# Kernel tuning notes

Measured on AMD Instinct MI355X. Metric: run time of the kernel, lower is better.

The kernel has to match this reference:

```python
import jax, jax.numpy as jnp
import numpy as np
import math

H = 2
NC, NPR = 100000, 50000
IN, HID, OUT = 128, 128, 16
E1, E2 = 300000, 300000
D = HID // H


def _segment_softmax(scores, seg, num_segments):
    m = jax.ops.segment_max(scores, seg, num_segments=num_segments)
    m = jax.lax.stop_gradient(jnp.where(jnp.isfinite(m), m, 0.0))
    e = jnp.exp(scores - m[seg])
    s = jax.ops.segment_sum(e, seg, num_segments=num_segments)
    return e / (s[seg] + 1e-16)


def _hgt_layer(xc, xp, ecp_s, ecp_d, epc_s, epc_d, prm):
    (wc, bc, wp, bp, acp, mcp, pcp, apc, mpc, ppc,
     owc, obc, owp, obp, sc, sp) = prm
    Nc, Np = xc.shape[0], xp.shape[0]

    def kqv(x, w, b):
        t = x @ w + b
        k, q, v = jnp.split(t, 3, axis=1)
        d = k.shape[1] // H
        return k.reshape(-1, H, d), q.reshape(-1, H, d), v.reshape(-1, H, d)

    kc, qc, vc = kqv(xc, wc, bc)
    kp, qp, vp = kqv(xp, wp, bp)
    d = kc.shape[-1]
    # relation-specific transforms applied to source-node keys/values (a_rel / m_rel)
    k_cp = jnp.einsum('nhd,hde->nhe', kc, acp)
    v_cp = jnp.einsum('nhd,hde->nhe', vc, mcp)
    k_pc = jnp.einsum('nhd,hde->nhe', kp, apc)
    v_pc = jnp.einsum('nhd,hde->nhe', vp, mpc)
    # merged destination index space: customers [0,Nc), products [Nc,Nc+Np)
    q_all = jnp.concatenate([qc, qp], axis=0)
    kj = jnp.concatenate([k_cp[ecp_s], k_pc[epc_s]], axis=0)  # [E,H,D] per-edge gather
    vj = jnp.concatenate([v_cp[ecp_s], v_pc[epc_s]], axis=0)
    dst = jnp.concatenate([ecp_d + Nc, epc_d], axis=0)
    prel = jnp.concatenate([jnp.broadcast_to(pcp, (ecp_s.shape[0], H)),
                            jnp.broadcast_to(ppc, (epc_s.shape[0], H))], axis=0)
    alpha = (q_all[dst] * kj).sum(-1) * prel / math.sqrt(d)  # [E,H]
    alpha = _segment_softmax(alpha, dst, Nc + Np)  # softmax over all incoming edges per dst node
    out = jax.ops.segment_sum(vj * alpha[..., None], dst, num_segments=Nc + Np)
    out = out.reshape(Nc + Np, H * d)

    def mix(o, x, ow, ob, s):
        o = jax.nn.gelu(o, approximate=False) @ ow + ob
        g = jax.nn.sigmoid(s)
        return g * o + (1.0 - g) * x

    return mix(out[:Nc], xc, owc, obc, sc), mix(out[Nc:], xp, owp, obp, sp)


def setup_inputs():
    key = jax.random.key(0)
    ks = list(jax.random.split(key, 64))
    it = iter(range(64))

    def nrm(shape, scale):
        return jax.random.normal(ks[next(it)], shape, dtype=jnp.float32) * scale

    inp = {}
    inp['xc'] = nrm((NC, IN), 1.0)
    inp['xp'] = nrm((NPR, IN), 1.0)
    for l in (1, 2):
        fin = IN if l == 1 else HID
        inp[f'w{l}c'] = nrm((fin, 3 * HID), 0.08)
        inp[f'b{l}c'] = jnp.zeros((3 * HID,), jnp.float32)
        inp[f'w{l}p'] = nrm((fin, 3 * HID), 0.08)
        inp[f'b{l}p'] = jnp.zeros((3 * HID,), jnp.float32)
        for et in ('cp', 'pc'):
            inp[f'a{l}{et}'] = nrm((H, D, D), 0.125)
            inp[f'm{l}{et}'] = nrm((H, D, D), 0.125)
            inp[f'p{l}{et}'] = jnp.ones((H,), jnp.float32)
        inp[f'ow{l}c'] = nrm((HID, HID), 0.08)
        inp[f'ob{l}c'] = jnp.zeros((HID,), jnp.float32)
        inp[f'ow{l}p'] = nrm((HID, HID), 0.08)
        inp[f'ob{l}p'] = jnp.zeros((HID,), jnp.float32)
        inp[f's{l}c'] = jnp.ones((1,), jnp.float32)
        inp[f's{l}p'] = jnp.ones((1,), jnp.float32)
    inp['wl'] = nrm((HID, OUT), 0.08)
    inp['bl'] = jnp.zeros((OUT,), jnp.float32)
    inp['ecp_s'] = jax.random.randint(ks[next(it)], (E1,), 0, NC, dtype=jnp.int32)
    inp['ecp_d'] = jax.random.randint(ks[next(it)], (E1,), 0, NPR, dtype=jnp.int32)
    inp['epc_s'] = jax.random.randint(ks[next(it)], (E2,), 0, NPR, dtype=jnp.int32)
    inp['epc_d'] = jax.random.randint(ks[next(it)], (E2,), 0, NC, dtype=jnp.int32)
    return inp


def reference(xc, xp, w1c, b1c, w1p, b1p, a1cp, m1cp, p1cp, a1pc, m1pc, p1pc, ow1c, ob1c, ow1p, ob1p, s1c, s1p, w2c, b2c, w2p, b2p, a2cp, m2cp, p2cp, a2pc, m2pc, p2pc, ow2c, ob2c, ow2p, ob2p, s2c, s2p, wl, bl, ecp_s, ecp_d, epc_s, epc_d):
    oc, op = _hgt_layer(xc, xp, ecp_s, ecp_d, epc_s, epc_d,
                        (w1c, b1c, w1p, b1p, a1cp, m1cp, p1cp, a1pc, m1pc, p1pc, ow1c, ob1c, ow1p, ob1p, s1c, s1p))
    oc, op = jax.nn.relu(oc), jax.nn.relu(op)
    oc, op = _hgt_layer(oc, op, ecp_s, ecp_d, epc_s, epc_d,
                        (w2c, b2c, w2p, b2p, a2cp, m2cp, p2cp, a2pc, m2pc, p2pc, ow2c, ob2c, ow2p, ob2p, s2c, s2p))
    return oc @ wl + bl
```

## Files before the change

### kernel.cpp

```cpp
#include <hip/hip_runtime.h>

typedef __attribute__((ext_vector_type(8))) short s16x8;
typedef __attribute__((ext_vector_type(4))) float f32x4;

constexpr int kNC = 100000;
constexpr int kNP = 50000;
constexpr int kNT = kNC + kNP;
constexpr int kE1 = 300000;
constexpr int kE2 = 300000;
constexpr int kCAP = 32;

__device__ __forceinline__ float geluf(float x) {
    return 0.5f * x * (1.0f + erff(x * 0.7071067811865475f));
}
__device__ __forceinline__ unsigned short f2bf(float f) {
    unsigned int u = __float_as_uint(f);
    u += 0x7fffu + ((u >> 16) & 1u);
    return (unsigned short)(u >> 16);
}
__device__ __forceinline__ float bf2f(unsigned short s) {
    return __uint_as_float(((unsigned int)s) << 16);
}

__global__ void fold_k(const float* __restrict__ w, const float* __restrict__ b,
                       const float* __restrict__ ar, const float* __restrict__ mr,
                       float* __restrict__ weff, float* __restrict__ beff) {
    int col = blockIdx.x;
    int i = threadIdx.x;
    float acc, bacc;
    if (col >= 128 && col < 256) {
        acc = w[i * 384 + col];
        bacc = b[col];
    } else {
        const float* rel = (col < 128) ? ar : mr;
        int base = (col < 128) ? 0 : 256;
        int c = col - base;
        int h = c >> 6, j = c & 63;
        acc = 0.0f; bacc = 0.0f;
        for (int d = 0; d < 64; ++d) {
            float rv = rel[(h * 64 + d) * 64 + j];
            acc  = fmaf(w[i * 384 + base + h * 64 + d], rv, acc);
            bacc = fmaf(b[base + h * 64 + d], rv, bacc);
        }
    }
    weff[i * 384 + col] = acc;
    if (i == 0) beff[col] = bacc;
}

struct Job {
    const float* W;
    const float* bias;
    const void* A;
    const float* Xres;
    const float* sgate;
    void* out;
    int M;
    int ldb;
    int abf16;
    int bf16out;
};

template<int PRO, int EPI, int RELU, int FINAL>
__global__ __launch_bounds__(256) void gemm128(
    Job j0, Job j1, Job j2, Job j3, Job j4, Job j5,
    const float* __restrict__ wl, const float* __restrict__ bl)
{
    Job J;
    switch (blockIdx.y) {
        case 0: J = j0; break;
        case 1: J = j1; break;
        case 2: J = j2; break;
        case 3: J = j3; break;
        case 4: J = j4; break;
        default: J = j5; break;
    }
    const int row0 = blockIdx.x * 128;
    if (row0 >= J.M) return;

    constexpr int LDE = 36;
    constexpr int LDP = 132;
    constexpr int NSM = FINAL ? (128 * LDP) : (2 * 128 * LDE);
    __shared__ unsigned short sm[NSM];
    unsigned short* As = sm;
    unsigned short* Bs = sm + 128 * LDE;

    const int t = threadIdx.x;
    const int lane = t & 63;
    const int w = t >> 6;
    const int l15 = lane & 15, l4 = lane >> 4;
    const int M = J.M;

    f32x4 acc[2][8];
    #pragma unroll
    for (int n = 0; n < 8; ++n) {
        float bv = J.bias[n * 16 + l15];
        acc[0][n] = f32x4{bv, bv, bv, bv};
        acc[1][n] = acc[0][n];
    }

    for (int kc = 0; kc < 4; ++kc) {
        const int k0 = kc * 32;
        uint2 pa[4];
        #pragma unroll
        for (int i = 0; i < 4; ++i) {
            int idx = i * 256 + t;
            int r = idx >> 3, kq = idx & 7;
            int gr = row0 + r;
            if (J.abf16) {
                ushort4 rv = {0, 0, 0, 0};
                if (gr < M) rv = *(const ushort4*)((const unsigned short*)J.A + (size_t)gr * 128 + k0 + kq * 4);
                if (PRO) {
                    pa[i].x = (unsigned)f2bf(geluf(bf2f(rv.x))) | ((unsigned)f2bf(geluf(bf2f(rv.y))) << 16);
                    pa[i].y = (unsigned)f2bf(geluf(bf2f(rv.z))) | ((unsigned)f2bf(geluf(bf2f(rv.w))) << 16);
                } else {
                    pa[i].x = (unsigned)rv.x | ((unsigned)rv.y << 16);
                    pa[i].y = (unsigned)rv.z | ((unsigned)rv.w << 16);
                }
            } else {
                float4 v = make_float4(0.f, 0.f, 0.f, 0.f);
                if (gr < M) v = *(const float4*)((const float*)J.A + (size_t)gr * 128 + k0 + kq * 4);
                if (PRO) { v.x = geluf(v.x); v.y = geluf(v.y); v.z = geluf(v.z); v.w = geluf(v.w); }
                pa[i].x = (unsigned)f2bf(v.x) | ((unsigned)f2bf(v.y) << 16);
                pa[i].y = (unsigned)f2bf(v.z) | ((unsigned)f2bf(v.w) << 16);
            }
        }
        float wv[4][4];
        #pragma unroll
        for (int i = 0; i < 4; ++i) {
            int idx = i * 256 + t;
            int c = idx & 127, kq = idx >> 7;
            #pragma unroll
            for (int k2 = 0; k2 < 4; ++k2)
                wv[i][k2] = J.W[(size_t)(k0 + kq * 4 + k2) * J.ldb + c];
        }
        if (kc) __syncthreads();
        #pragma unroll
        for (int i = 0; i < 4; ++i) {
            int idx = i * 256 + t;
            int r = idx >> 3, kq = idx & 7;
            *(uint2*)&As[r * LDE + kq * 4] = pa[i];
            int c = idx & 127, kq2 = idx >> 7;
            uint2 pb;
            pb.x = (unsigned)f2bf(wv[i][0]) | ((unsigned)f2bf(wv[i][1]) << 16);
            pb.y = (unsigned)f2bf(wv[i][2]) | ((unsigned)f2bf(wv[i][3]) << 16);
            *(uint2*)&Bs[c * LDE + kq2 * 4] = pb;
        }
        __syncthreads();

        union FR { uint2 u[2]; s16x8 v; };
        FR af[2];
        #pragma unroll
        for (int m = 0; m < 2; ++m) {
            const unsigned short* p = &As[(w * 32 + m * 16 + l15) * LDE + l4 * 4];
            af[m].u[0] = *(const uint2*)p;
            af[m].u[1] = *(const uint2*)(p + 16);
        }
        #pragma unroll
        for (int n = 0; n < 8; ++n) {
            const unsigned short* p = &Bs[(n * 16 + l15) * LDE + l4 * 4];
            FR bfr;
            bfr.u[0] = *(const uint2*)p;
            bfr.u[1] = *(const uint2*)(p + 16);
            acc[0][n] = __builtin_amdgcn_mfma_f32_16x16x32_bf16(af[0].v, bfr.v, acc[0][n], 0, 0, 0);
            acc[1][n] = __builtin_amdgcn_mfma_f32_16x16x32_bf16(af[1].v, bfr.v, acc[1][n], 0, 0, 0);
        }
    }

    float g = 0.f, omg = 0.f;
    if (EPI == 1) { g = 1.0f / (1.0f + expf(-J.sgate[0])); omg = 1.0f - g; }

    if (FINAL) __syncthreads();

    #pragma unroll
    for (int m = 0; m < 2; ++m) {
        #pragma unroll
        for (int r = 0; r < 4; ++r) {
            int lr = w * 32 + m * 16 + l4 * 4 + r;
            int gr = row0 + lr;
            bool ok = gr < M;
            #pragma unroll
            for (int n = 0; n < 8; ++n) {
                float v = acc[m][n][r];
                if (EPI == 1) {
                    float xv = ok ? J.Xres[(size_t)gr * 128 + n * 16 + l15] : 0.f;
                    v = g * v + omg * xv;
                    if (RELU) v = fmaxf(v, 0.0f);
                }
                if (FINAL) {
                    sm[lr * LDP + n * 16 + l15] = f2bf(v);
                } else if (ok) {
                    if (J.bf16out)
                        ((unsigned short*)J.out)[(size_t)gr * 128 + n * 16 + l15] = f2bf(v);
                    else
                        ((float*)J.out)[(size_t)gr * 128 + n * 16 + l15] = v;
                }
            }
        }
    }

    if (FINAL) {
        union FR { uint2 u[2]; s16x8 v; };
        f32x4 facc[2];
        float bv = bl[l15];
        facc[0] = f32x4{bv, bv, bv, bv};
        facc[1] = facc[0];
        #pragma unroll
        for (int kc2 = 0; kc2 < 4; ++kc2) {
            FR bfr;
            #pragma unroll
            for (int h = 0; h < 2; ++h) {
                float f0 = wl[(size_t)(kc2 * 32 + h * 16 + l4 * 4 + 0) * 16 + l15];
                float f1 = wl[(size_t)(kc2 * 32 + h * 16 + l4 * 4 + 1) * 16 + l15];
                float f2 = wl[(size_t)(kc2 * 32 + h * 16 + l4 * 4 + 2) * 16 + l15];
                float f3 = wl[(size_t)(kc2 * 32 + h * 16 + l4 * 4 + 3) * 16 + l15];
                bfr.u[h].x = (unsigned)f2bf(f0) | ((unsigned)f2bf(f1) << 16);
                bfr.u[h].y = (unsigned)f2bf(f2) | ((unsigned)f2bf(f3) << 16);
            }
            #pragma unroll
            for (int m = 0; m < 2; ++m) {
                FR afr;
                const unsigned short* p = &sm[(w * 32 + m * 16 + l15) * LDP + kc2 * 32 + l4 * 4];
                afr.u[0] = *(const uint2*)p;
                afr.u[1] = *(const uint2*)(p + 16);
                facc[m] = __builtin_amdgcn_mfma_f32_16x16x32_bf16(afr.v, bfr.v, facc[m], 0, 0, 0);
            }
        }
        #pragma unroll
        for (int m = 0; m < 2; ++m) {
            #pragma unroll
            for (int r = 0; r < 4; ++r) {
                int gr = row0 + w * 32 + m * 16 + l4 * 4 + r;
                if (gr < M) ((float*)J.out)[(size_t)gr * 16 + l15] = facc[m][r];
            }
        }
    }
}

__global__ __launch_bounds__(256) void build_bucket(
    const int* __restrict__ src, const int* __restrict__ dst, int E,
    int* __restrict__ cnt, int* __restrict__ bucket)
{
    int e = blockIdx.x * 256 + threadIdx.x;
    if (e >= E) return;
    int d = dst[e];
    int slot = atomicAdd(&cnt[d], 1);
    if (slot < kCAP) bucket[(size_t)d * kCAP + slot] = src[e];
}

__global__ __launch_bounds__(256) void fused_attn2(
    int nA, const int* __restrict__ cntA, const int* __restrict__ bucketA,
    const unsigned short* __restrict__ kA, const unsigned short* __restrict__ vA,
    unsigned short* __restrict__ qoA, const float* __restrict__ prelA,
    int nB, const int* __restrict__ cntB, const int* __restrict__ bucketB,
    const unsigned short* __restrict__ kB, const unsigned short* __restrict__ vB,
    unsigned short* __restrict__ qoB, const float* __restrict__ prelB)
{
    int wid = (blockIdx.x * 256 + threadIdx.x) >> 6;
    int lane = threadIdx.x & 63;
    const int* cnt; const int* bucket; const unsigned short* ks; const unsigned short* vs;
    unsigned short* qo; const float* prel;
    if (wid < nA) {
        cnt = cntA; bucket = bucketA; ks = kA; vs = vA; qo = qoA; prel = prelA;
    } else {
        wid -= nA;
        if (wid >= nB) return;
        cnt = cntB; bucket = bucketB; ks = kB; vs = vB; qo = qoB; prel = prelB;
    }
    int deg = cnt[wid];
    if (deg > kCAP) deg = kCAP;
    int mys = (lane < deg) ? bucket[(size_t)wid * kCAP + lane] : 0;
    unsigned int qv = *(const unsigned int*)(qo + (size_t)wid * 128 + lane * 2);
    float qx = bf2f((unsigned short)qv), qy = bf2f((unsigned short)(qv >> 16));
    float ph = prel[lane >> 5] * 0.125f;
    float m = -3.4e38f, ss = 0.f, o0 = 0.f, o1 = 0.f;
    for (int i = 0; i < deg; ++i) {
        int s = __shfl(mys, i);
        unsigned int kk = *(const unsigned int*)(ks + (size_t)s * 128 + lane * 2);
        float p = qx * bf2f((unsigned short)kk) + qy * bf2f((unsigned short)(kk >> 16));
        p += __shfl_xor(p, 1);
        p += __shfl_xor(p, 2);
        p += __shfl_xor(p, 4);
        p += __shfl_xor(p, 8);
        p += __shfl_xor(p, 16);
        float lg = p * ph;
        float mn = fmaxf(m, lg);
        float sc = __expf(m - mn);
        float wgt = __expf(lg - mn);
        unsigned int vv = *(const unsigned int*)(vs + (size_t)s * 128 + lane * 2);
        ss = ss * sc + wgt;
        o0 = o0 * sc + wgt * bf2f((unsigned short)vv);
        o1 = o1 * sc + wgt * bf2f((unsigned short)(vv >> 16));
        m = mn;
    }
    float r = 1.0f / (ss + 1e-16f);
    unsigned int ov = (unsigned)f2bf(o0 * r) | ((unsigned)f2bf(o1 * r) << 16);
    *(unsigned int*)(qo + (size_t)wid * 128 + lane * 2) = ov;
}

extern "C" void kernel_launch(void* const* d_in, const int* in_sizes, int n_in,
                              void* d_out, int out_size, void* d_ws, size_t ws_size,
                              hipStream_t stream)
{
    const float* xc  = (const float*)d_in[0];
    const float* xp  = (const float*)d_in[1];
    const float* w1c = (const float*)d_in[2];
    const float* b1c = (const float*)d_in[3];
    const float* w1p = (const float*)d_in[4];
    const float* b1p = (const float*)d_in[5];
    const float* a1cp= (const float*)d_in[6];
    const float* m1cp= (const float*)d_in[7];
    const float* p1cp= (const float*)d_in[8];
    const float* a1pc= (const float*)d_in[9];
    const float* m1pc= (const float*)d_in[10];
    const float* p1pc= (const float*)d_in[11];
    const float* ow1c= (const float*)d_in[12];
    const float* ob1c= (const float*)d_in[13];
    const float* ow1p= (const float*)d_in[14];
    const float* ob1p= (const float*)d_in[15];
    const float* s1c = (const float*)d_in[16];
    const float* s1p = (const float*)d_in[17];
    const float* w2c = (const float*)d_in[18];
    const float* b2c = (const float*)d_in[19];
    const float* w2p = (const float*)d_in[20];
    const float* b2p = (const float*)d_in[21];
    const float* a2pc= (const float*)d_in[25];
    const float* m2pc= (const float*)d_in[26];
    const float* p2pc= (const float*)d_in[27];
    const float* ow2c= (const float*)d_in[28];
    const float* ob2c= (const float*)d_in[29];
    const float* s2c = (const float*)d_in[32];
    const float* wl  = (const float*)d_in[34];
    const float* bl  = (const float*)d_in[35];
    const int* ecp_s = (const int*)d_in[36];
    const int* ecp_d = (const int*)d_in[37];
    const int* epc_s = (const int*)d_in[38];
    const int* epc_d = (const int*)d_in[39];
    float* outF = (float*)d_out;
    (void)in_sizes; (void)n_in; (void)out_size; (void)ws_size;

    char* ws = (char*)d_ws;
    size_t off = 0;
    auto take = [&](size_t bytes) { char* p = ws + off; off += (bytes + 255) & ~(size_t)255; return p; };
    char* R0 = take((size_t)kNC * 128 * 4);
    unsigned short* kC = (unsigned short*)R0;
    unsigned short* vC = (unsigned short*)(R0 + (size_t)kNC * 128 * 2);
    float* hc = (float*)R0;
    char* R1 = take((size_t)kNP * 128 * 4);
    unsigned short* kP = (unsigned short*)R1;
    unsigned short* vP = (unsigned short*)(R1 + (size_t)kNP * 128 * 2);
    unsigned short* kP2 = kP;
    unsigned short* vP2 = vP;
    unsigned short* qAll = (unsigned short*)take((size_t)kNT * 128 * 2);
    unsigned short* qC = qAll;
    unsigned short* qP = qAll + (size_t)kNC * 128;
    unsigned short* hp = (unsigned short*)take((size_t)kNP * 128 * 2);
    int* cntP = (int*)take((size_t)kNP * 4);
    int* cntC = (int*)take((size_t)kNC * 4);
    int* bucketP = (int*)take((size_t)kNP * kCAP * 4);
    int* bucketC = (int*)take((size_t)kNC * kCAP * 4);
    float* wec = (float*)take((size_t)128 * 384 * 4);
    float* bec = (float*)take((size_t)384 * 4);
    float* wep = (float*)take((size_t)128 * 384 * 4);
    float* bep = (float*)take((size_t)384 * 4);

    auto cdiv = [](int a, int b) { return (a + b - 1) / b; };
    dim3 blk(256);
    const int gx = cdiv(kNC, 128);
    const float* nf = nullptr;

    hipMemsetAsync(cntP, 0, (size_t)kNP * 4, stream);
    hipMemsetAsync(cntC, 0, (size_t)kNC * 4, stream);
    hipLaunchKernelGGL(build_bucket, dim3(cdiv(kE1, 256)), blk, 0, stream, ecp_s, ecp_d, kE1, cntP, bucketP);
    hipLaunchKernelGGL(build_bucket, dim3(cdiv(kE2, 256)), blk, 0, stream, epc_s, epc_d, kE2, cntC, bucketC);

    hipLaunchKernelGGL(fold_k, dim3(384), dim3(128), 0, stream, w1c, b1c, a1cp, m1cp, wec, bec);
    hipLaunchKernelGGL(fold_k, dim3(384), dim3(128), 0, stream, w1p, b1p, a1pc, m1pc, wep, bep);

    Job jkC = { wec + 0,   bec + 0,   xc, nf, nf, (void*)kC, kNC, 384, 0, 1 };
    Job jqC = { wec + 128, bec + 128, xc, nf, nf, (void*)qC, kNC, 384, 0, 1 };
    Job jvC = { wec + 256, bec + 256, xc, nf, nf, (void*)vC, kNC, 384, 0, 1 };
    Job jkP = { wep + 0,   bep + 0,   xp, nf, nf, (void*)kP, kNP, 384, 0, 1 };
    Job jqP = { wep + 128, bep + 128, xp, nf, nf, (void*)qP, kNP, 384, 0, 1 };
    Job jvP = { wep + 256, bep + 256, xp, nf, nf, (void*)vP, kNP, 384, 0, 1 };
    hipLaunchKernelGGL((gemm128<0,0,0,0>), dim3(gx, 6), blk, 0, stream,
                       jkC, jqC, jvC, jkP, jqP, jvP, nf, nf);

    hipLaunchKernelGGL(fused_attn2, dim3(cdiv(kNP + kNC, 4)), blk, 0, stream,
                       kNP, cntP, bucketP, kC, vC, qP, p1cp,
                       kNC, cntC, bucketC, kP, vP, qC, p1pc);

    Job jmC = { ow1c, ob1c, qC, xc, s1c, (void*)hc, kNC, 128, 1, 0 };
    Job jmP = { ow1p, ob1p, qP, xp, s1p, (void*)hp, kNP, 128, 1, 1 };
    hipLaunchKernelGGL((gemm128<1,1,1,0>), dim3(gx, 2), blk, 0, stream,
                       jmC, jmP, jmC, jmC, jmC, jmC, nf, nf);

    hipLaunchKernelGGL(fold_k, dim3(384), dim3(128), 0, stream, w2p, b2p, a2pc, m2pc, wep, bep);
    Job jk2 = { wep + 0,   bep + 0,   hp, nf, nf, (void*)kP2, kNP, 384, 1, 1 };
    Job jv2 = { wep + 256, bep + 256, hp, nf, nf, (void*)vP2, kNP, 384, 1, 1 };
    Job jq2 = { w2c + 128, b2c + 128, hc, nf, nf, (void*)qC,  kNC, 384, 0, 1 };
    hipLaunchKernelGGL((gemm128<0,0,0,0>), dim3(gx, 3), blk, 0, stream,
                       jk2, jv2, jq2, jk2, jk2, jk2, nf, nf);

    hipLaunchKernelGGL(fused_attn2, dim3(cdiv(kNC, 4)), blk, 0, stream,
                       kNC, cntC, bucketC, kP2, vP2, qC, p2pc,
                       0, cntC, bucketC, kP2, vP2, qC, p2pc);

    Job jf = { ow2c, ob2c, qC, hc, s2c, (void*)outF, kNC, 128, 1, 0 };
    hipLaunchKernelGGL((gemm128<1,1,0,1>), dim3(gx, 1), blk, 0, stream,
                       jf, jf, jf, jf, jf, jf, wl, bl);
}
```

Before: 434.8 us.

## Stage A tile once and compute K/Q/V outputs per block; two-pass softmax

The GEMM kernel now loads the full 128x128 A tile into shared memory once and loops over up to three weight matrices (K, Q, V) in the same block. Before, separate blocks per output each re-read and re-converted the input rows. Grids become 1D with per-job block offsets, so no blocks are launched for product jobs past their row count. The attention kernel swaps online-softmax rescaling for a two-pass scheme: logits are kept per lane, the max and sum are taken with shuffles, then a plain weighted accumulation runs. The cost is larger shared memory (about 73KB per block), which lowers occupancy, plus a serial weight load per output.

```diff
diff --git a/kernel.cpp b/kernel.cpp
--- a/kernel.cpp
+++ b/kernel.cpp
@@ -48,160 +48,146 @@
 }
 
 struct Job {
-    const float* W;
-    const float* bias;
     const void* A;
     const float* Xres;
     const float* sgate;
-    void* out;
-    int M;
-    int ldb;
-    int abf16;
-    int bf16out;
+    int M, ldb, abf16, nout, blk0;
+    const float* W0; const float* b0; void* out0; int bf0;
+    const float* W1; const float* b1; void* out1; int bf1;
+    const float* W2; const float* b2; void* out2; int bf2;
 };
 
-template<int PRO, int EPI, int RELU, int FINAL>
-__global__ __launch_bounds__(256) void gemm128(
-    Job j0, Job j1, Job j2, Job j3, Job j4, Job j5,
-    const float* __restrict__ wl, const float* __restrict__ bl)
+template<int PRO, int EPI, int RELU, int FINAL, int NJ>
+__global__ __launch_bounds__(256) void gemmN(
+    Job j0, Job j1, const float* __restrict__ wl, const float* __restrict__ blv)
 {
-    Job J;
-    switch (blockIdx.y) {
-        case 0: J = j0; break;
-        case 1: J = j1; break;
-        case 2: J = j2; break;
-        case 3: J = j3; break;
-        case 4: J = j4; break;
-        default: J = j5; break;
-    }
-    const int row0 = blockIdx.x * 128;
-    if (row0 >= J.M) return;
-
-    constexpr int LDE = 36;
-    constexpr int LDP = 132;
-    constexpr int NSM = FINAL ? (128 * LDP) : (2 * 128 * LDE);
-    __shared__ unsigned short sm[NSM];
-    unsigned short* As = sm;
-    unsigned short* Bs = sm + 128 * LDE;
+    Job J = j0;
+    if (NJ > 1 && (int)blockIdx.x >= j1.blk0) J = j1;
+    const int row0 = ((int)blockIdx.x - J.blk0) * 128;
+    const int M = J.M;
+    if (row0 >= M) return;
+
+    constexpr int CH = 128 * 36;
+    __shared__ unsigned short As[4 * CH];
+    __shared__ unsigned short Bs[4 * CH];
 
     const int t = threadIdx.x;
-    const int lane = t & 63;
-    const int w = t >> 6;
+    const int lane = t & 63, w = t >> 6;
     const int l15 = lane & 15, l4 = lane >> 4;
-    const int M = J.M;
-
-    f32x4 acc[2][8];
+
     #pragma unroll
-    for (int n = 0; n < 8; ++n) {
-        float bv = J.bias[n * 16 + l15];
-        acc[0][n] = f32x4{bv, bv, bv, bv};
-        acc[1][n] = acc[0][n];
-    }
-
-    for (int kc = 0; kc < 4; ++kc) {
-        const int k0 = kc * 32;
-        uint2 pa[4];
-        #pragma unroll
-        for (int i = 0; i < 4; ++i) {
-            int idx = i * 256 + t;
-            int r = idx >> 3, kq = idx & 7;
-            int gr = row0 + r;
-            if (J.abf16) {
-                ushort4 rv = {0, 0, 0, 0};
-                if (gr < M) rv = *(const ushort4*)((const unsigned short*)J.A + (size_t)gr * 128 + k0 + kq * 4);
-                if (PRO) {
-                    pa[i].x = (unsigned)f2bf(geluf(bf2f(rv.x))) | ((unsigned)f2bf(geluf(bf2f(rv.y))) << 16);
-                    pa[i].y = (unsigned)f2bf(geluf(bf2f(rv.z))) | ((unsigned)f2bf(geluf(bf2f(rv.w))) << 16);
-                } else {
-                    pa[i].x = (unsigned)rv.x | ((unsigned)rv.y << 16);
-                    pa[i].y = (unsigned)rv.z | ((unsigned)rv.w << 16);
+    for (int i = 0; i < 16; ++i) {
+        int q = i * 256 + t;
+        int kc = q >> 10, rem = q & 1023, r = rem >> 3, kq = rem & 7;
+        int gr = row0 + r;
+        uint2 pa;
+        if (J.abf16) {
+            ushort4 rv = {0, 0, 0, 0};
+            if (gr < M) rv = *(const ushort4*)((const unsigned short*)J.A + (size_t)gr * 128 + kc * 32 + kq * 4);
+            if (PRO) {
+                pa.x = (unsigned)f2bf(geluf(bf2f(rv.x))) | ((unsigned)f2bf(geluf(bf2f(rv.y))) << 16);
+                pa.y = (unsigned)f2bf(geluf(bf2f(rv.z))) | ((unsigned)f2bf(geluf(bf2f(rv.w))) << 16);
+            } else {
+                pa.x = (unsigned)rv.x | ((unsigned)rv.y << 16);
+                pa.y = (unsigned)rv.z | ((unsigned)rv.w << 16);
+            }
+        } else {
+            float4 v = make_float4(0.f, 0.f, 0.f, 0.f);
+            if (gr < M) v = *(const float4*)((const float*)J.A + (size_t)gr * 128 + kc * 32 + kq * 4);
+            if (PRO) { v.x = geluf(v.x); v.y = geluf(v.y); v.z = geluf(v.z); v.w = geluf(v.w); }
+            pa.x = (unsigned)f2bf(v.x) | ((unsigned)f2bf(v.y) << 16);
+            pa.y = (unsigned)f2bf(v.z) | ((unsigned)f2bf(v.w) << 16);
+        }
+        *(uint2*)&As[kc * CH + r * 36 + kq * 4] = pa;
+    }
+
+    float gg = 0.f, omg = 0.f;
+    if (EPI == 1) { gg = 1.0f / (1.0f + expf(-J.sgate[0])); omg = 1.0f - gg; }
+
+    union FR { uint2 u[2]; s16x8 v; };
+
+    #pragma unroll
+    for (int o = 0; o < 3; ++o) {
+        if (o >= J.nout) break;
+        const float* W  = (o == 0) ? J.W0 : (o == 1 ? J.W1 : J.W2);
+        const float* bi = (o == 0) ? J.b0 : (o == 1 ? J.b1 : J.b2);
+        void* outp      = (o == 0) ? J.out0 : (o == 1 ? J.out1 : J.out2);
+        const int bfo   = (o == 0) ? J.bf0 : (o == 1 ? J.bf1 : J.bf2);
+
+        if (o) __syncthreads();
+        #pragma unroll
+        for (int i = 0; i < 16; ++i) {
+            int q = i * 256 + t;
+            int kc = q >> 10, rem = q & 1023, kq = rem >> 7, c = rem & 127;
+            int kb = kc * 32 + kq * 4;
+            float f0 = W[(size_t)(kb + 0) * J.ldb + c];
+            float f1 = W[(size_t)(kb + 1) * J.ldb + c];
+            float f2 = W[(size_t)(kb + 2) * J.ldb + c];
+            float f3 = W[(size_t)(kb + 3) * J.ldb + c];
+            uint2 pb;
+            pb.x = (unsigned)f2bf(f0) | ((unsigned)f2bf(f1) << 16);
+            pb.y = (unsigned)f2bf(f2) | ((unsigned)f2bf(f3) << 16);
+            *(uint2*)&Bs[kc * CH + c * 36 + kq * 4] = pb;
+        }
+        __syncthreads();
+
+        f32x4 acc[2][8];
+        #pragma unroll
+        for (int n = 0; n < 8; ++n) {
+            float bv = bi[n * 16 + l15];
+            acc[0][n] = f32x4{bv, bv, bv, bv};
+            acc[1][n] = acc[0][n];
+        }
+        #pragma unroll
+        for (int kc = 0; kc < 4; ++kc) {
+            FR af[2];
+            #pragma unroll
+            for (int m = 0; m < 2; ++m) {
+                const unsigned short* p = &As[kc * CH + (w * 32 + m * 16 + l15) * 36 + l4 * 4];
+                af[m].u[0] = *(const uint2*)p;
+                af[m].u[1] = *(const uint2*)(p + 16);
+            }
+            #pragma unroll
+            for (int n = 0; n < 8; ++n) {
+                const unsigned short* p = &Bs[kc * CH + (n * 16 + l15) * 36 + l4 * 4];
+                FR bfr;
+                bfr.u[0] = *(const uint2*)p;
+                bfr.u[1] = *(const uint2*)(p + 16);
+                acc[0][n] = __builtin_amdgcn_mfma_f32_16x16x32_bf16(af[0].v, bfr.v, acc[0][n], 0, 0, 0);
+                acc[1][n] = __builtin_amdgcn_mfma_f32_16x16x32_bf16(af[1].v, bfr.v, acc[1][n], 0, 0, 0);
+            }
+        }
+
+        if (FINAL) __syncthreads();
+        #pragma unroll
+        for (int m = 0; m < 2; ++m) {
+            #pragma unroll
+            for (int r = 0; r < 4; ++r) {
+                int lr = w * 32 + m * 16 + l4 * 4 + r;
+                int gr = row0 + lr;
+                bool ok = gr < M;
+                #pragma unroll
+                for (int n = 0; n < 8; ++n) {
+                    float v = acc[m][n][r];
+                    if (EPI == 1) {
+                        float xv = ok ? J.Xres[(size_t)gr * 128 + n * 16 + l15] : 0.f;
+                        v = gg * v + omg * xv;
+                        if (RELU) v = fmaxf(v, 0.0f);
+                    }
+                    if (FINAL) {
+                        As[lr * 132 + n * 16 + l15] = f2bf(v);
+                    } else if (ok) {
+                        if (bfo) ((unsigned short*)outp)[(size_t)gr * 128 + n * 16 + l15] = f2bf(v);
+                        else     ((float*)outp)[(size_t)gr * 128 + n * 16 + l15] = v;
+                    }
                 }
-            } else {
-                float4 v = make_float4(0.f, 0.f, 0.f, 0.f);
-                if (gr < M) v = *(const float4*)((const float*)J.A + (size_t)gr * 128 + k0 + kq * 4);
-                if (PRO) { v.x = geluf(v.x); v.y = geluf(v.y); v.z = geluf(v.z); v.w = geluf(v.w); }
-                pa[i].x = (unsigned)f2bf(v.x) | ((unsigned)f2bf(v.y) << 16);
-                pa[i].y = (unsigned)f2bf(v.z) | ((unsigned)f2bf(v.w) << 16);
-            }
-        }
-        float wv[4][4];
-        #pragma unroll
-        for (int i = 0; i < 4; ++i) {
-            int idx = i * 256 + t;
-            int c = idx & 127, kq = idx >> 7;
-            #pragma unroll
-            for (int k2 = 0; k2 < 4; ++k2)
-                wv[i][k2] = J.W[(size_t)(k0 + kq * 4 + k2) * J.ldb + c];
-        }
-        if (kc) __syncthreads();
-        #pragma unroll
-        for (int i = 0; i < 4; ++i) {
-            int idx = i * 256 + t;
-            int r = idx >> 3, kq = idx & 7;
-            *(uint2*)&As[r * LDE + kq * 4] = pa[i];
-            int c = idx & 127, kq2 = idx >> 7;
-            uint2 pb;
-            pb.x = (unsigned)f2bf(wv[i][0]) | ((unsigned)f2bf(wv[i][1]) << 16);
-            pb.y = (unsigned)f2bf(wv[i][2]) | ((unsigned)f2bf(wv[i][3]) << 16);
-            *(uint2*)&Bs[c * LDE + kq2 * 4] = pb;
-        }
-        __syncthreads();
-
-        union FR { uint2 u[2]; s16x8 v; };
-        FR af[2];
-        #pragma unroll
-        for (int m = 0; m < 2; ++m) {
-            const unsigned short* p = &As[(w * 32 + m * 16 + l15) * LDE + l4 * 4];
-            af[m].u[0] = *(const uint2*)p;
-            af[m].u[1] = *(const uint2*)(p + 16);
-        }
-        #pragma unroll
-        for (int n = 0; n < 8; ++n) {
-            const unsigned short* p = &Bs[(n * 16 + l15) * LDE + l4 * 4];
-            FR bfr;
-            bfr.u[0] = *(const uint2*)p;
-            bfr.u[1] = *(const uint2*)(p + 16);
-            acc[0][n] = __builtin_amdgcn_mfma_f32_16x16x32_bf16(af[0].v, bfr.v, acc[0][n], 0, 0, 0);
-            acc[1][n] = __builtin_amdgcn_mfma_f32_16x16x32_bf16(af[1].v, bfr.v, acc[1][n], 0, 0, 0);
-        }
-    }
-
-    float g = 0.f, omg = 0.f;
-    if (EPI == 1) { g = 1.0f / (1.0f + expf(-J.sgate[0])); omg = 1.0f - g; }
-
-    if (FINAL) __syncthreads();
-
-    #pragma unroll
-    for (int m = 0; m < 2; ++m) {
-        #pragma unroll
-        for (int r = 0; r < 4; ++r) {
-            int lr = w * 32 + m * 16 + l4 * 4 + r;
-            int gr = row0 + lr;
-            bool ok = gr < M;
-            #pragma unroll
-            for (int n = 0; n < 8; ++n) {
-                float v = acc[m][n][r];
-                if (EPI == 1) {
-                    float xv = ok ? J.Xres[(size_t)gr * 128 + n * 16 + l15] : 0.f;
-                    v = g * v + omg * xv;
-                    if (RELU) v = fmaxf(v, 0.0f);
-                }
-                if (FINAL) {
-                    sm[lr * LDP + n * 16 + l15] = f2bf(v);
-                } else if (ok) {
-                    if (J.bf16out)
-                        ((unsigned short*)J.out)[(size_t)gr * 128 + n * 16 + l15] = f2bf(v);
-                    else
-                        ((float*)J.out)[(size_t)gr * 128 + n * 16 + l15] = v;
-                }
             }
         }
     }
 
     if (FINAL) {
-        union FR { uint2 u[2]; s16x8 v; };
         f32x4 facc[2];
-        float bv = bl[l15];
+        float bv = blv[l15];
         facc[0] = f32x4{bv, bv, bv, bv};
         facc[1] = facc[0];
         #pragma unroll
@@ -219,7 +205,7 @@
             #pragma unroll
             for (int m = 0; m < 2; ++m) {
                 FR afr;
-                const unsigned short* p = &sm[(w * 32 + m * 16 + l15) * LDP + kc2 * 32 + l4 * 4];
+                const unsigned short* p = &As[(w * 32 + m * 16 + l15) * 132 + kc2 * 32 + l4 * 4];
                 afr.u[0] = *(const uint2*)p;
                 afr.u[1] = *(const uint2*)(p + 16);
                 facc[m] = __builtin_amdgcn_mfma_f32_16x16x32_bf16(afr.v, bfr.v, facc[m], 0, 0, 0);
@@ -230,7 +216,7 @@
             #pragma unroll
             for (int r = 0; r < 4; ++r) {
                 int gr = row0 + w * 32 + m * 16 + l4 * 4 + r;
-                if (gr < M) ((float*)J.out)[(size_t)gr * 16 + l15] = facc[m][r];
+                if (gr < M) ((float*)J.out0)[(size_t)gr * 16 + l15] = facc[m][r];
             }
         }
     }
@@ -268,11 +254,13 @@
     }
     int deg = cnt[wid];
     if (deg > kCAP) deg = kCAP;
+    const int lane31 = lane & 31;
     int mys = (lane < deg) ? bucket[(size_t)wid * kCAP + lane] : 0;
     unsigned int qv = *(const unsigned int*)(qo + (size_t)wid * 128 + lane * 2);
     float qx = bf2f((unsigned short)qv), qy = bf2f((unsigned short)(qv >> 16));
     float ph = prel[lane >> 5] * 0.125f;
-    float m = -3.4e38f, ss = 0.f, o0 = 0.f, o1 = 0.f;
+
+    float mx = -3.4e38f, mylg = -3.4e38f;
     for (int i = 0; i < deg; ++i) {
         int s = __shfl(mys, i);
         unsigned int kk = *(const unsigned int*)(ks + (size_t)s * 128 + lane * 2);
@@ -283,17 +271,27 @@
         p += __shfl_xor(p, 8);
         p += __shfl_xor(p, 16);
         float lg = p * ph;
-        float mn = fmaxf(m, lg);
-        float sc = __expf(m - mn);
-        float wgt = __expf(lg - mn);
+        if (lane31 == i) mylg = lg;
+        mx = fmaxf(mx, lg);
+    }
+    float wgt = (lane31 < deg) ? __expf(mylg - mx) : 0.f;
+    float ssum = wgt;
+    ssum += __shfl_xor(ssum, 1);
+    ssum += __shfl_xor(ssum, 2);
+    ssum += __shfl_xor(ssum, 4);
+    ssum += __shfl_xor(ssum, 8);
+    ssum += __shfl_xor(ssum, 16);
+    float rr = 1.0f / (ssum + 1e-16f);
+
+    float o0 = 0.f, o1 = 0.f;
+    for (int i = 0; i < deg; ++i) {
+        int s = __shfl(mys, i);
+        float wi = __shfl(wgt, (lane & 32) + i);
         unsigned int vv = *(const unsigned int*)(vs + (size_t)s * 128 + lane * 2);
-        ss = ss * sc + wgt;
-        o0 = o0 * sc + wgt * bf2f((unsigned short)vv);
-        o1 = o1 * sc + wgt * bf2f((unsigned short)(vv >> 16));
-        m = mn;
-    }
-    float r = 1.0f / (ss + 1e-16f);
-    unsigned int ov = (unsigned)f2bf(o0 * r) | ((unsigned)f2bf(o1 * r) << 16);
+        o0 = fmaf(wi, bf2f((unsigned short)vv), o0);
+        o1 = fmaf(wi, bf2f((unsigned short)(vv >> 16)), o1);
+    }
+    unsigned int ov = (unsigned)f2bf(o0 * rr) | ((unsigned)f2bf(o1 * rr) << 16);
     *(unsigned int*)(qo + (size_t)wid * 128 + lane * 2) = ov;
 }
 
@@ -365,7 +363,8 @@
 
     auto cdiv = [](int a, int b) { return (a + b - 1) / b; };
     dim3 blk(256);
-    const int gx = cdiv(kNC, 128);
+    const int nbC = cdiv(kNC, 128);
+    const int nbP = cdiv(kNP, 128);
     const float* nf = nullptr;
 
     hipMemsetAsync(cntP, 0, (size_t)kNP * 4, stream);
@@ -376,36 +375,45 @@
     hipLaunchKernelGGL(fold_k, dim3(384), dim3(128), 0, stream, w1c, b1c, a1cp, m1cp, wec, bec);
     hipLaunchKernelGGL(fold_k, dim3(384), dim3(128), 0, stream, w1p, b1p, a1pc, m1pc, wep, bep);
 
-    Job jkC = { wec + 0,   bec + 0,   xc, nf, nf, (void*)kC, kNC, 384, 0, 1 };
-    Job jqC = { wec + 128, bec + 128, xc, nf, nf, (void*)qC, kNC, 384, 0, 1 };
-    Job jvC = { wec + 256, bec + 256, xc, nf, nf, (void*)vC, kNC, 384, 0, 1 };
-    Job jkP = { wep + 0,   bep + 0,   xp, nf, nf, (void*)kP, kNP, 384, 0, 1 };
-    Job jqP = { wep + 128, bep + 128, xp, nf, nf, (void*)qP, kNP, 384, 0, 1 };
-    Job jvP = { wep + 256, bep + 256, xp, nf, nf, (void*)vP, kNP, 384, 0, 1 };
-    hipLaunchKernelGGL((gemm128<0,0,0,0>), dim3(gx, 6), blk, 0, stream,
-                       jkC, jqC, jvC, jkP, jqP, jvP, nf, nf);
+    Job jC = { xc, nf, nf, kNC, 384, 0, 3, 0,
+               wec + 0,   bec + 0,   (void*)kC, 1,
+               wec + 128, bec + 128, (void*)qC, 1,
+               wec + 256, bec + 256, (void*)vC, 1 };
+    Job jP = { xp, nf, nf, kNP, 384, 0, 3, nbC,
+               wep + 0,   bep + 0,   (void*)kP, 1,
+               wep + 128, bep + 128, (void*)qP, 1,
+               wep + 256, bep + 256, (void*)vP, 1 };
+    hipLaunchKernelGGL((gemmN<0,0,0,0,2>), dim3(nbC + nbP), blk, 0, stream, jC, jP, nf, nf);
 
     hipLaunchKernelGGL(fused_attn2, dim3(cdiv(kNP + kNC, 4)), blk, 0, stream,
                        kNP, cntP, bucketP, kC, vC, qP, p1cp,
                        kNC, cntC, bucketC, kP, vP, qC, p1pc);
 
-    Job jmC = { ow1c, ob1c, qC, xc, s1c, (void*)hc, kNC, 128, 1, 0 };
-    Job jmP = { ow1p, ob1p, qP, xp, s1p, (void*)hp, kNP, 128, 1, 1 };
-    hipLaunchKernelGGL((gemm128<1,1,1,0>), dim3(gx, 2), blk, 0, stream,
-                       jmC, jmP, jmC, jmC, jmC, jmC, nf, nf);
+    Job mC = { qC, xc, s1c, kNC, 128, 1, 1, 0,
+               ow1c, ob1c, (void*)hc, 0,
+               nf, nf, nullptr, 0, nf, nf, nullptr, 0 };
+    Job mP = { qP, xp, s1p, kNP, 128, 1, 1, nbC,
+               ow1p, ob1p, (void*)hp, 1,
+               nf, nf, nullptr, 0, nf, nf, nullptr, 0 };
+    hipLaunchKernelGGL((gemmN<1,1,1,0,2>), dim3(nbC + nbP), blk, 0, stream, mC, mP, nf, nf);
 
     hipLaunchKernelGGL(fold_k, dim3(384), dim3(128), 0, stream, w2p, b2p, a2pc, m2pc, wep, bep);
-    Job jk2 = { wep + 0,   bep + 0,   hp, nf, nf, (void*)kP2, kNP, 384, 1, 1 };
-    Job jv2 = { wep + 256, bep + 256, hp, nf, nf, (void*)vP2, kNP, 384, 1, 1 };
-    Job jq2 = { w2c + 128, b2c + 128, hc, nf, nf, (void*)qC,  kNC, 384, 0, 1 };
-    hipLaunchKernelGGL((gemm128<0,0,0,0>), dim3(gx, 3), blk, 0, stream,
-                       jk2, jv2, jq2, jk2, jk2, jk2, nf, nf);
+
+    Job j2p = { hp, nf, nf, kNP, 384, 1, 2, 0,
+                wep + 0,   bep + 0,   (void*)kP2, 1,
+                wep + 256, bep + 256, (void*)vP2, 1,
+                nf, nf, nullptr, 0 };
+    Job j2c = { hc, nf, nf, kNC, 384, 0, 1, nbP,
+                w2c + 128, b2c + 128, (void*)qC, 1,
+                nf, nf, nullptr, 0, nf, nf, nullptr, 0 };
+    hipLaunchKernelGGL((gemmN<0,0,0,0,2>), dim3(nbP + nbC), blk, 0, stream, j2p, j2c, nf, nf);
 
     hipLaunchKernelGGL(fused_attn2, dim3(cdiv(kNC, 4)), blk, 0, stream,
                        kNC, cntC, bucketC, kP2, vP2, qC, p2pc,
                        0, cntC, bucketC, kP2, vP2, qC, p2pc);
 
-    Job jf = { ow2c, ob2c, qC, hc, s2c, (void*)outF, kNC, 128, 1, 0 };
-    hipLaunchKernelGGL((gemm128<1,1,0,1>), dim3(gx, 1), blk, 0, stream,
-                       jf, jf, jf, jf, jf, jf, wl, bl);
-}
+    Job jf = { qC, hc, s2c, kNC, 128, 1, 1, 0,
+               ow2c, ob2c, (void*)outF, 0,
+               nf, nf, nullptr, 0, nf, nf, nullptr, 0 };
+    hipLaunchKernelGGL((gemmN<1,1,0,1,1>), dim3(nbC), blk, 0, stream, jf, jf, wl, bl);
+}
```

New measurement: 657.0 us. 51.1% more time.

## Pre-convert inputs to bf16 and use two-pass softmax in attention

Applied to the files above, without the earlier changes.

Adds a kernel that converts xc and xp to bf16 once, so the first fused KQV GEMM reads bf16 activations (flag set to 1) instead of fp32 six times across its job columns. The attention kernel replaces the online-softmax recurrence with two passes: first compute all logits and the max, then do a warp-level sum and a weighted V accumulation with broadcast weights. The first change adds an extra conversion launch and workspace. The second removes per-edge exp rescaling but issues the neighbour index shuffle twice.

```diff
diff --git a/kernel.cpp b/kernel.cpp
--- a/kernel.cpp
+++ b/kernel.cpp
@@ -20,6 +20,19 @@
 }
 __device__ __forceinline__ float bf2f(unsigned short s) {
     return __uint_as_float(((unsigned int)s) << 16);
+}
+
+__global__ __launch_bounds__(256) void cvt_bf16(
+    const float* __restrict__ in, unsigned short* __restrict__ out, int n8)
+{
+    int i = blockIdx.x * 256 + threadIdx.x;
+    if (i >= n8) return;
+    float4 a = *(const float4*)(in + (size_t)i * 8);
+    float4 b = *(const float4*)(in + (size_t)i * 8 + 4);
+    ushort4 o0 = { f2bf(a.x), f2bf(a.y), f2bf(a.z), f2bf(a.w) };
+    ushort4 o1 = { f2bf(b.x), f2bf(b.y), f2bf(b.z), f2bf(b.w) };
+    *(ushort4*)(out + (size_t)i * 8) = o0;
+    *(ushort4*)(out + (size_t)i * 8 + 4) = o1;
 }
 
 __global__ void fold_k(const float* __restrict__ w, const float* __restrict__ b,
@@ -268,11 +281,13 @@
     }
     int deg = cnt[wid];
     if (deg > kCAP) deg = kCAP;
+    const int lane31 = lane & 31;
     int mys = (lane < deg) ? bucket[(size_t)wid * kCAP + lane] : 0;
     unsigned int qv = *(const unsigned int*)(qo + (size_t)wid * 128 + lane * 2);
     float qx = bf2f((unsigned short)qv), qy = bf2f((unsigned short)(qv >> 16));
     float ph = prel[lane >> 5] * 0.125f;
-    float m = -3.4e38f, ss = 0.f, o0 = 0.f, o1 = 0.f;
+
+    float mx = -3.4e38f, mylg = -3.4e38f;
     for (int i = 0; i < deg; ++i) {
         int s = __shfl(mys, i);
         unsigned int kk = *(const unsigned int*)(ks + (size_t)s * 128 + lane * 2);
@@ -283,17 +298,27 @@
         p += __shfl_xor(p, 8);
         p += __shfl_xor(p, 16);
         float lg = p * ph;
-        float mn = fmaxf(m, lg);
-        float sc = __expf(m - mn);
-        float wgt = __expf(lg - mn);
+        if (lane31 == i) mylg = lg;
+        mx = fmaxf(mx, lg);
+    }
+    float wgt = (lane31 < deg) ? __expf(mylg - mx) : 0.f;
+    float ssum = wgt;
+    ssum += __shfl_xor(ssum, 1);
+    ssum += __shfl_xor(ssum, 2);
+    ssum += __shfl_xor(ssum, 4);
+    ssum += __shfl_xor(ssum, 8);
+    ssum += __shfl_xor(ssum, 16);
+    float rr = 1.0f / (ssum + 1e-16f);
+
+    float o0 = 0.f, o1 = 0.f;
+    for (int i = 0; i < deg; ++i) {
+        int s = __shfl(mys, i);
+        float wi = __shfl(wgt, (lane & 32) + i);
         unsigned int vv = *(const unsigned int*)(vs + (size_t)s * 128 + lane * 2);
-        ss = ss * sc + wgt;
-        o0 = o0 * sc + wgt * bf2f((unsigned short)vv);
-        o1 = o1 * sc + wgt * bf2f((unsigned short)(vv >> 16));
-        m = mn;
-    }
-    float r = 1.0f / (ss + 1e-16f);
-    unsigned int ov = (unsigned)f2bf(o0 * r) | ((unsigned)f2bf(o1 * r) << 16);
+        o0 = fmaf(wi, bf2f((unsigned short)vv), o0);
+        o1 = fmaf(wi, bf2f((unsigned short)(vv >> 16)), o1);
+    }
+    unsigned int ov = (unsigned)f2bf(o0 * rr) | ((unsigned)f2bf(o1 * rr) << 16);
     *(unsigned int*)(qo + (size_t)wid * 128 + lane * 2) = ov;
 }
 
@@ -362,6 +387,8 @@
     float* bec = (float*)take((size_t)384 * 4);
     float* wep = (float*)take((size_t)128 * 384 * 4);
     float* bep = (float*)take((size_t)384 * 4);
+    unsigned short* xcb = (unsigned short*)take((size_t)kNC * 128 * 2);
+    unsigned short* xpb = (unsigned short*)take((size_t)kNP * 128 * 2);
 
     auto cdiv = [](int a, int b) { return (a + b - 1) / b; };
     dim3 blk(256);
@@ -373,15 +400,18 @@
     hipLaunchKernelGGL(build_bucket, dim3(cdiv(kE1, 256)), blk, 0, stream, ecp_s, ecp_d, kE1, cntP, bucketP);
     hipLaunchKernelGGL(build_bucket, dim3(cdiv(kE2, 256)), blk, 0, stream, epc_s, epc_d, kE2, cntC, bucketC);
 
+    hipLaunchKernelGGL(cvt_bf16, dim3(cdiv(kNC * 16, 256)), blk, 0, stream, xc, xcb, kNC * 16);
+    hipLaunchKernelGGL(cvt_bf16, dim3(cdiv(kNP * 16, 256)), blk, 0, stream, xp, xpb, kNP * 16);
+
     hipLaunchKernelGGL(fold_k, dim3(384), dim3(128), 0, stream, w1c, b1c, a1cp, m1cp, wec, bec);
     hipLaunchKernelGGL(fold_k, dim3(384), dim3(128), 0, stream, w1p, b1p, a1pc, m1pc, wep, bep);
 
-    Job jkC = { wec + 0,   bec + 0,   xc, nf, nf, (void*)kC, kNC, 384, 0, 1 };
-    Job jqC = { wec + 128, bec + 128, xc, nf, nf, (void*)qC, kNC, 384, 0, 1 };
-    Job jvC = { wec + 256, bec + 256, xc, nf, nf, (void*)vC, kNC, 384, 0, 1 };
-    Job jkP = { wep + 0,   bep + 0,   xp, nf, nf, (void*)kP, kNP, 384, 0, 1 };
-    Job jqP = { wep + 128, bep + 128, xp, nf, nf, (void*)qP, kNP, 384, 0, 1 };
-    Job jvP = { wep + 256, bep + 256, xp, nf, nf, (void*)vP, kNP, 384, 0, 1 };
+    Job jkC = { wec + 0,   bec + 0,   xcb, nf, nf, (void*)kC, kNC, 384, 1, 1 };
+    Job jqC = { wec + 128, bec + 128, xcb, nf, nf, (void*)qC, kNC, 384, 1, 1 };
+    Job jvC = { wec + 256, bec + 256, xcb, nf, nf, (void*)vC, kNC, 384, 1, 1 };
+    Job jkP = { wep + 0,   bep + 0,   xpb, nf, nf, (void*)kP, kNP, 384, 1, 1 };
+    Job jqP = { wep + 128, bep + 128, xpb, nf, nf, (void*)qP, kNP, 384, 1, 1 };
+    Job jvP = { wep + 256, bep + 256, xpb, nf, nf, (void*)vP, kNP, 384, 1, 1 };
     hipLaunchKernelGGL((gemm128<0,0,0,0>), dim3(gx, 6), blk, 0, stream,
                        jkC, jqC, jvC, jkP, jqP, jvP, nf, nf);
 
```

Result: slower. 501.0 us (+15.2%).
